# Kernel tuning notes

Measured on AMD Instinct MI355X. Metric: run time of the kernel, lower is better.

## Reference

```python
import jax, jax.numpy as jnp
import numpy as np

B, K, D = 8, 256, 768      # batch, num proposals, appearance_feature_dim
DK = 96                    # key_feature_dim
DG = 96                    # geo_feature_dim
NR = 8                     # n_relations (NR*DK == D required by residual add)


def setup_inputs() -> dict:
    key = jax.random.key(0)
    ks = jax.random.split(key, 10)
    s = 0.02
    return {
        "f_a": jax.random.normal(ks[0], (B, K, D), jnp.float32),
        "position_embedding": jax.random.uniform(ks[1], (B, K, K, DG), jnp.float32),
        # stacked per-head parameters (NR heads)
        "WG_w": jax.random.normal(ks[2], (NR, DG), jnp.float32) * s,
        "WG_b": jnp.zeros((NR,), jnp.float32),
        "WK_w": jax.random.normal(ks[3], (NR, D, DK), jnp.float32) * s,
        "WK_b": jnp.zeros((NR, DK), jnp.float32),
        "WQ_w": jax.random.normal(ks[4], (NR, D, DK), jnp.float32) * s,
        "WQ_b": jnp.zeros((NR, DK), jnp.float32),
        "WV_w": jax.random.normal(ks[5], (NR, D, DK), jnp.float32) * s,
        "WV_b": jnp.zeros((NR, DK), jnp.float32),
    }


def reference(f_a, position_embedding, WG_w, WG_b, WK_w, WK_b, WQ_w, WQ_b, WV_w, WV_b):
    # Per-head projections, all heads at once: [B, H, K, DK]
    k = jnp.einsum('bkd,hde->bhke', f_a, WK_w) + WK_b[:, None, :]
    q = jnp.einsum('bkd,hde->bhke', f_a, WQ_w) + WQ_b[:, None, :]
    v = jnp.einsum('bkd,hde->bhke', f_a, WV_w) + WV_b[:, None, :]
    # scaled_dot[b,h,m,n] = <k_m, q_n> / sqrt(DK)  (matches w_k.view(B,K,1,dk)*w_q.view(B,1,K,dk))
    scores = jnp.einsum('bhme,bhne->bhmn', k, q) * (1.0 / np.sqrt(DK)).astype(np.float32)
    # geometric bias: relu(WG(pe)) -> [B,H,K,K]
    w_g = jax.nn.relu(jnp.einsum('bmng,hg->bhmn', position_embedding, WG_w) + WG_b[:, None, None])
    logits = jnp.log(jnp.clip(w_g, 1e-6)) + scores
    # torch Softmax(dim=1) on [B,K,K] -> normalize over m axis (axis=2 here)
    attn = jax.nn.softmax(logits, axis=2)
    # output[b,n,:] = sum_m attn[b,h,m,n] * v[b,h,m,:], heads concatenated on feature dim
    out = jnp.einsum('bhmn,bhmd->bnhd', attn, v).reshape(f_a.shape[0], f_a.shape[1], -1)
    return out + f_a  # concat + f_a residual from RelationalProposalModule
```

## Files before the change

kernel.cpp:

```cpp
#include <hip/hip_runtime.h>

#define DD   768
#define NH   8
#define DKh  96
#define NROW 2048
#define NCOL 2304

typedef __attribute__((ext_vector_type(8))) short short8;
typedef __attribute__((ext_vector_type(4))) float f32x4;

__device__ __forceinline__ unsigned short f2bf(float x) {
    union { float f; unsigned int u; } v; v.f = x;
    unsigned int r = v.u + 0x7FFFu + ((v.u >> 16) & 1u);
    return (unsigned short)(r >> 16);
}

__global__ __launch_bounds__(256) void k_cvt_a(const float* __restrict__ fa,
                                               unsigned short* __restrict__ abf) {
    int idx = blockIdx.x * 256 + threadIdx.x;
    float4 v = ((const float4*)fa)[idx];
    ushort4 o;
    o.x = f2bf(v.x); o.y = f2bf(v.y); o.z = f2bf(v.z); o.w = f2bf(v.w);
    ((ushort4*)abf)[idx] = o;
}

__global__ __launch_bounds__(256) void k_cvt_w(const float* __restrict__ wk,
                                               const float* __restrict__ wq,
                                               const float* __restrict__ wv,
                                               unsigned short* __restrict__ wbf) {
    __shared__ float ls[64 * 97];
    int pid = blockIdx.x / 12;
    int db  = blockIdx.x % 12;
    int p = pid >> 3, h = pid & 7;
    const float* src = (p == 0 ? wk : p == 1 ? wq : wv) + h * DD * DKh + db * 64 * DKh;
    int t = threadIdx.x;
#pragma unroll
    for (int i = 0; i < 24; ++i) {
        int f = t + 256 * i;
        int dl = f / 96, e = f - dl * 96;
        ls[dl * 97 + e] = src[f];
    }
    __syncthreads();
    unsigned short* dst = wbf + (p * 768 + h * 96) * DD + db * 64;
#pragma unroll
    for (int i = 0; i < 24; ++i) {
        int f = t + 256 * i;
        int e = f >> 6, dl = f & 63;
        dst[e * DD + dl] = f2bf(ls[dl * 97 + e]);
    }
}

__global__ __launch_bounds__(256) void k_proj(const unsigned short* __restrict__ abf,
                                              const unsigned short* __restrict__ wbf,
                                              const float* __restrict__ wkb,
                                              const float* __restrict__ wqb,
                                              const float* __restrict__ wvb,
                                              unsigned short* __restrict__ kb,
                                              unsigned short* __restrict__ qb,
                                              unsigned short* __restrict__ vt) {
    int w = threadIdx.x >> 6, lane = threadIdx.x & 63;
    int lrow = lane & 15, quad = lane >> 4;
    int rt = blockIdx.x / 9, cg = blockIdx.x % 9;
    int r0 = rt * 16;
    int c0 = cg * 256 + w * 64;
    f32x4 z = {0.f, 0.f, 0.f, 0.f};
    f32x4 acc[4] = {z, z, z, z};
    for (int kk = 0; kk < DD; kk += 32) {
        short8 a = *(const short8*)(abf + (r0 + lrow) * DD + kk + quad * 8);
#pragma unroll
        for (int tt = 0; tt < 4; ++tt) {
            short8 b = *(const short8*)(wbf + (c0 + tt * 16 + lrow) * DD + kk + quad * 8);
            acc[tt] = __builtin_amdgcn_mfma_f32_16x16x32_bf16(a, b, acc[tt], 0, 0, 0);
        }
    }
    int rbase = r0 + quad * 4;
    int b_ = rbase >> 8, mbase = rbase & 255;
#pragma unroll
    for (int tt = 0; tt < 4; ++tt) {
        int cc = c0 + tt * 16 + lrow;
        int p = cc / 768, rm = cc - p * 768;
        int h = rm / 96,  e = rm - h * 96;
        float bias = (p == 0 ? wkb : p == 1 ? wqb : wvb)[h * 96 + e];
        if (p == 2) {
            ushort4 v4;
            v4.x = f2bf(acc[tt][0] + bias);
            v4.y = f2bf(acc[tt][1] + bias);
            v4.z = f2bf(acc[tt][2] + bias);
            v4.w = f2bf(acc[tt][3] + bias);
            *(ushort4*)(vt + ((b_ * 8 + h) * 96 + e) * 256 + mbase) = v4;
        } else {
            float sc = (p == 1) ? 0.10206207261596577f : 1.0f;
            unsigned short* dst = (p == 0 ? kb : qb) + ((b_ * 8 + h) * 256 + mbase) * 96 + e;
#pragma unroll
            for (int r = 0; r < 4; ++r)
                dst[r * 96] = f2bf((acc[tt][r] + bias) * sc);
        }
    }
}

__global__ __launch_bounds__(256) void k_wg(const float* __restrict__ pe,
                                            const float* __restrict__ wgw,
                                            const float* __restrict__ wgb,
                                            float* __restrict__ L) {
    __shared__ float ps[64 * 97];
    int bi = blockIdx.x;
    int b = bi >> 10, rem = bi & 1023;
    int m = rem >> 2, nb = rem & 3;
    int n0 = nb * 64;
    int t = threadIdx.x;
    const float* src = pe + ((b * 256 + m) * 256 + n0) * 96;
#pragma unroll
    for (int i = 0; i < 24; ++i) {
        int f = t + 256 * i;
        int r = f / 96, e = f - r * 96;
        ps[r * 97 + e] = src[f];
    }
    __syncthreads();
    int wq_ = __builtin_amdgcn_readfirstlane((int)(threadIdx.x >> 6));
    const float* w0 = wgw + (2 * wq_) * 96;
    const float* w1 = w0 + 96;
    float acc0 = wgb[2 * wq_], acc1 = wgb[2 * wq_ + 1];
    int n = t & 63;
    const float* row = ps + n * 97;
#pragma unroll
    for (int g = 0; g < 96; ++g) {
        float pv = row[g];
        acc0 = fmaf(pv, w0[g], acc0);
        acc1 = fmaf(pv, w1[g], acc1);
    }
    float l0 = __logf(fmaxf(acc0, 1e-6f));
    float l1 = __logf(fmaxf(acc1, 1e-6f));
    int h0 = 2 * wq_;
    L[((b * 8 + h0) * 256 + m) * 256 + n0 + n] = l0;
    L[((b * 8 + h0 + 1) * 256 + m) * 256 + n0 + n] = l1;
}

__global__ __launch_bounds__(256) void k_score(const unsigned short* __restrict__ kb,
                                               const unsigned short* __restrict__ qb,
                                               float* __restrict__ L) {
    int w = threadIdx.x >> 6, lane = threadIdx.x & 63;
    int lrow = lane & 15, quad = lane >> 4;
    int tid = blockIdx.x * 4 + w;
    int bh = tid >> 8, rem = tid & 255;
    int mt = rem >> 4, nt = rem & 15;
    int m0 = mt * 16, n0 = nt * 16;
    f32x4 acc = {0.f, 0.f, 0.f, 0.f};
    const unsigned short* ka = kb + (bh * 256 + m0 + lrow) * 96 + quad * 8;
    const unsigned short* qa = qb + (bh * 256 + n0 + lrow) * 96 + quad * 8;
#pragma unroll
    for (int kk = 0; kk < 96; kk += 32) {
        short8 a = *(const short8*)(ka + kk);
        short8 b = *(const short8*)(qa + kk);
        acc = __builtin_amdgcn_mfma_f32_16x16x32_bf16(a, b, acc, 0, 0, 0);
    }
    float* lp = L + (bh * 256 + m0 + quad * 4) * 256 + n0 + lrow;
#pragma unroll
    for (int r = 0; r < 4; ++r)
        lp[r * 256] += acc[r];
}

__global__ __launch_bounds__(256) void k_softmax(const float* __restrict__ L,
                                                 unsigned short* __restrict__ pt) {
    __shared__ float Ps[32 * 264];
    __shared__ float inv_s[32];
    int bh = blockIdx.x >> 3, nbk = blockIdx.x & 7;
    int n0 = nbk * 32;
    int t = threadIdx.x;
    int nl = t >> 3, j = t & 7;
    const float* base = L + bh * 65536 + n0 + nl;
    float mx = -3.4e38f;
    for (int m0 = 0; m0 < 256; m0 += 8)
        mx = fmaxf(mx, base[(m0 + j) * 256]);
    mx = fmaxf(mx, __shfl_xor(mx, 1));
    mx = fmaxf(mx, __shfl_xor(mx, 2));
    mx = fmaxf(mx, __shfl_xor(mx, 4));
    float sum = 0.f;
    for (int m0 = 0; m0 < 256; m0 += 8) {
        float v = base[(m0 + j) * 256];
        float e = __expf(v - mx);
        sum += e;
        Ps[nl * 264 + m0 + j] = e;
    }
    sum += __shfl_xor(sum, 1);
    sum += __shfl_xor(sum, 2);
    sum += __shfl_xor(sum, 4);
    if (j == 0) inv_s[nl] = 1.0f / sum;
    __syncthreads();
    unsigned short* dst = pt + (bh * 256 + n0) * 256;
#pragma unroll 4
    for (int i = 0; i < 32; ++i)
        dst[i * 256 + t] = f2bf(Ps[i * 264 + t] * inv_s[i]);
}

__global__ __launch_bounds__(256) void k_attnv(const unsigned short* __restrict__ pt,
                                               const unsigned short* __restrict__ vt,
                                               const float* __restrict__ fa,
                                               float* __restrict__ out) {
    int w = threadIdx.x >> 6, lane = threadIdx.x & 63;
    int lrow = lane & 15, quad = lane >> 4;
    int tid = blockIdx.x * 4 + w;
    int bh = tid / 96, rem = tid - bh * 96;
    int nt = rem / 6, et = rem - nt * 6;
    int n0 = nt * 16, e0 = et * 16;
    int b_ = bh >> 3, h = bh & 7;
    f32x4 acc = {0.f, 0.f, 0.f, 0.f};
    const unsigned short* pa = pt + (bh * 256 + n0 + lrow) * 256 + quad * 8;
    const unsigned short* va = vt + (bh * 96 + e0 + lrow) * 256 + quad * 8;
#pragma unroll
    for (int mk = 0; mk < 256; mk += 32) {
        short8 a = *(const short8*)(pa + mk);
        short8 b = *(const short8*)(va + mk);
        acc = __builtin_amdgcn_mfma_f32_16x16x32_bf16(a, b, acc, 0, 0, 0);
    }
    int idx = (b_ * 256 + n0 + quad * 4) * 768 + h * 96 + e0 + lrow;
#pragma unroll
    for (int r = 0; r < 4; ++r)
        out[idx + r * 768] = acc[r] + fa[idx + r * 768];
}

extern "C" void kernel_launch(void* const* d_in, const int* in_sizes, int n_in,
                              void* d_out, int out_size, void* d_ws, size_t ws_size,
                              hipStream_t stream) {
    const float* fa  = (const float*)d_in[0];
    const float* pe  = (const float*)d_in[1];
    const float* wgw = (const float*)d_in[2];
    const float* wgb = (const float*)d_in[3];
    const float* wkw = (const float*)d_in[4];
    const float* wkb = (const float*)d_in[5];
    const float* wqw = (const float*)d_in[6];
    const float* wqb = (const float*)d_in[7];
    const float* wvw = (const float*)d_in[8];
    const float* wvb = (const float*)d_in[9];
    float* out = (float*)d_out;
    char* ws = (char*)d_ws;
    unsigned short* abf = (unsigned short*)(ws);
    unsigned short* wbf = (unsigned short*)(ws + 3145728);
    unsigned short* kb  = (unsigned short*)(ws + 6684672);
    unsigned short* qb  = (unsigned short*)(ws + 9830400);
    unsigned short* vt  = (unsigned short*)(ws + 12976128);
    float*          L   = (float*)(ws + 16121856);
    unsigned short* pt  = (unsigned short*)(ws + 32899072);

    k_cvt_a  <<<1536, 256, 0, stream>>>(fa, abf);
    k_cvt_w  <<< 288, 256, 0, stream>>>(wkw, wqw, wvw, wbf);
    k_proj   <<<1152, 256, 0, stream>>>(abf, wbf, wkb, wqb, wvb, kb, qb, vt);
    k_wg     <<<8192, 256, 0, stream>>>(pe, wgw, wgb, L);
    k_score  <<<4096, 256, 0, stream>>>(kb, qb, L);
    k_softmax<<< 512, 256, 0, stream>>>(L, pt);
    k_attnv  <<<1536, 256, 0, stream>>>(pt, vt, fa, out);
}
```

Baseline: 407.9 us.

## Read position embedding once per pair for all heads in k_wg; retile k_proj

k_wg now assigns one thread per (b,m,n) pair. Each thread reads its 96-float embedding row with float4 loads and computes all 8 heads, instead of staging through LDS and having each wave handle two heads. This removes the LDS staging, the barrier and the redundant LDS reads, and quarters the grid. The catch is that each thread's row load is strided by 384 bytes, so coalescing is poor, and the weights are read from scalar or global memory. k_proj also changes its block tiling: four waves now share a 64-column weight slice across different rows rather than sharing rows.

Measured after the change: 419.5 us. 2.9% more time.

```diff
diff --git a/kernel.cpp b/kernel.cpp
--- a/kernel.cpp
+++ b/kernel.cpp
@@ -3,8 +3,6 @@
 #define DD   768
 #define NH   8
 #define DKh  96
-#define NROW 2048
-#define NCOL 2304
 
 typedef __attribute__((ext_vector_type(8))) short short8;
 typedef __attribute__((ext_vector_type(4))) float f32x4;
@@ -60,9 +58,9 @@
                                               unsigned short* __restrict__ vt) {
     int w = threadIdx.x >> 6, lane = threadIdx.x & 63;
     int lrow = lane & 15, quad = lane >> 4;
-    int rt = blockIdx.x / 9, cg = blockIdx.x % 9;
-    int r0 = rt * 16;
-    int c0 = cg * 256 + w * 64;
+    int rt = blockIdx.x / 36, cg = blockIdx.x % 36;
+    int r0 = rt * 64 + w * 16;
+    int c0 = cg * 64;
     f32x4 z = {0.f, 0.f, 0.f, 0.f};
     f32x4 acc[4] = {z, z, z, z};
     for (int kk = 0; kk < DD; kk += 32) {
@@ -102,37 +100,27 @@
                                             const float* __restrict__ wgw,
                                             const float* __restrict__ wgb,
                                             float* __restrict__ L) {
-    __shared__ float ps[64 * 97];
-    int bi = blockIdx.x;
-    int b = bi >> 10, rem = bi & 1023;
-    int m = rem >> 2, nb = rem & 3;
-    int n0 = nb * 64;
-    int t = threadIdx.x;
-    const float* src = pe + ((b * 256 + m) * 256 + n0) * 96;
-#pragma unroll
-    for (int i = 0; i < 24; ++i) {
-        int f = t + 256 * i;
-        int r = f / 96, e = f - r * 96;
-        ps[r * 97 + e] = src[f];
-    }
-    __syncthreads();
-    int wq_ = __builtin_amdgcn_readfirstlane((int)(threadIdx.x >> 6));
-    const float* w0 = wgw + (2 * wq_) * 96;
-    const float* w1 = w0 + 96;
-    float acc0 = wgb[2 * wq_], acc1 = wgb[2 * wq_ + 1];
-    int n = t & 63;
-    const float* row = ps + n * 97;
-#pragma unroll
-    for (int g = 0; g < 96; ++g) {
-        float pv = row[g];
-        acc0 = fmaf(pv, w0[g], acc0);
-        acc1 = fmaf(pv, w1[g], acc1);
-    }
-    float l0 = __logf(fmaxf(acc0, 1e-6f));
-    float l1 = __logf(fmaxf(acc1, 1e-6f));
-    int h0 = 2 * wq_;
-    L[((b * 8 + h0) * 256 + m) * 256 + n0 + n] = l0;
-    L[((b * 8 + h0 + 1) * 256 + m) * 256 + n0 + n] = l1;
+    int tid = blockIdx.x * 256 + threadIdx.x;
+    int n = tid & 255, m = (tid >> 8) & 255, b = tid >> 16;
+    const float4* row = (const float4*)(pe + (size_t)tid * 96);
+    float acc[8];
+#pragma unroll
+    for (int h = 0; h < 8; ++h) acc[h] = wgb[h];
+#pragma unroll
+    for (int g4 = 0; g4 < 24; ++g4) {
+        float4 v = row[g4];
+#pragma unroll
+        for (int h = 0; h < 8; ++h) {
+            acc[h] = fmaf(v.x, wgw[h * 96 + g4 * 4 + 0], acc[h]);
+            acc[h] = fmaf(v.y, wgw[h * 96 + g4 * 4 + 1], acc[h]);
+            acc[h] = fmaf(v.z, wgw[h * 96 + g4 * 4 + 2], acc[h]);
+            acc[h] = fmaf(v.w, wgw[h * 96 + g4 * 4 + 3], acc[h]);
+        }
+    }
+    int base = (b * 8 * 256 + m) * 256 + n;
+#pragma unroll
+    for (int h = 0; h < 8; ++h)
+        L[base + h * 65536] = __logf(fmaxf(acc[h], 1e-6f));
 }
 
 __global__ __launch_bounds__(256) void k_score(const unsigned short* __restrict__ kb,
@@ -244,7 +232,7 @@
     k_cvt_a  <<<1536, 256, 0, stream>>>(fa, abf);
     k_cvt_w  <<< 288, 256, 0, stream>>>(wkw, wqw, wvw, wbf);
     k_proj   <<<1152, 256, 0, stream>>>(abf, wbf, wkb, wqb, wvb, kb, qb, vt);
-    k_wg     <<<8192, 256, 0, stream>>>(pe, wgw, wgb, L);
+    k_wg     <<<2048, 256, 0, stream>>>(pe, wgw, wgb, L);
     k_score  <<<4096, 256, 0, stream>>>(kb, qb, L);
     k_softmax<<< 512, 256, 0, stream>>>(L, pt);
     k_attnv  <<<1536, 256, 0, stream>>>(pt, vt, fa, out);
```
